# Kernel optimization log

Hardware: AMD Instinct MI355X
Metric: run time of the kernel (lower is better)

## Reference

```python
import jax, jax.numpy as jnp
import numpy as np

# --- fake-quant helpers (Brevitas INT quantization, straight-through in bwd) ---

def quant_weight_2bit(w):
    # symmetric signed 2-bit, narrow range: integer levels {-1, 0, 1}
    qmax = 1.0
    s = jnp.max(jnp.abs(jax.lax.stop_gradient(w))) / qmax
    r = jnp.clip(jnp.round(w / s), -qmax, qmax) * s
    return w + jax.lax.stop_gradient(r - w)  # STE


def quant_relu_2bit(x, max_val=6.0):
    # unsigned 2-bit activation quant: levels {0, 1, 2, 3} scaled to [0, max_val]
    n = 3.0  # 2**2 - 1
    s = max_val / n
    y = jnp.clip(x, 0.0, max_val)  # relu + clamp at max_val
    r = jnp.round(y / s) * s
    return y + jax.lax.stop_gradient(r - y)  # STE


def conv3x3_same(x, w):
    # NCHW input, OIHW weight, stride 1, padding 1
    return jax.lax.conv_general_dilated(
        x, w, window_strides=(1, 1), padding=((1, 1), (1, 1)),
        dimension_numbers=("NCHW", "OIHW", "NCHW"))


def maxpool2x2(x):
    return jax.lax.reduce_window(
        x, -jnp.inf, jax.lax.max,
        window_dimensions=(1, 1, 2, 2), window_strides=(1, 1, 2, 2),
        padding="VALID")


def setup_inputs() -> dict:
    key = jax.random.key(0)
    k0, k1, k2, k3 = jax.random.split(key, 4)
    B = 32768
    x = jax.random.normal(k0, (B, 1, 28, 28), dtype=jnp.float32)
    w1 = jax.random.normal(k1, (4, 1, 3, 3), dtype=jnp.float32) * 0.3
    w2 = jax.random.normal(k2, (4, 4, 3, 3), dtype=jnp.float32) * 0.2
    wf = jax.random.normal(k3, (10, 4 * 7 * 7), dtype=jnp.float32) * 0.1
    return {"x": x, "w1": w1, "w2": w2, "wf": wf}


def reference(x, w1, w2, wf):
    h = conv3x3_same(x, quant_weight_2bit(w1))        # [B,4,28,28]
    h = quant_relu_2bit(h)
    h = maxpool2x2(h)                                  # [B,4,14,14]
    h = conv3x3_same(h, quant_weight_2bit(w2))         # [B,4,14,14]
    h = quant_relu_2bit(h)
    h = maxpool2x2(h)                                  # [B,4,7,7]
    h = h.reshape(h.shape[0], -1)                      # [B,196]
    return h @ quant_weight_2bit(wf).T                 # [B,10]
```

## Files before the change

kernel.cpp:

```cpp
#include <hip/hip_runtime.h>

#define WSF_W1Q  0
#define WSF_SF2  36
#define WSI_W2P  0
#define WSI_L1   36
#define WSI_L3   37
#define WSI_L5   38
#define WSI_WFP  40

#define TOL 1e-4f

__device__ __forceinline__ int dot4(int a, int b, int c) {
#if __has_builtin(__builtin_amdgcn_sdot4)
    return __builtin_amdgcn_sdot4(a, b, c, false);
#else
    c += (int)(signed char)(a)       * (int)(signed char)(b);
    c += (int)(signed char)(a >> 8)  * (int)(signed char)(b >> 8);
    c += (int)(signed char)(a >> 16) * (int)(signed char)(b >> 16);
    c += (int)(signed char)(a >> 24) * (int)(signed char)(b >> 24);
    return c;
#endif
}

__global__ void qweights_kernel(const float* __restrict__ w1,
                                const float* __restrict__ w2,
                                const float* __restrict__ wf,
                                float* __restrict__ wsf) {
    int* wsi = (int*)wsf + 64;
    __shared__ float red[256];
    const int tid = threadIdx.x;

    float m = 0.f;
    for (int i = tid; i < 36; i += 256) m = fmaxf(m, fabsf(w1[i]));
    red[tid] = m; __syncthreads();
    for (int s = 128; s > 0; s >>= 1) { if (tid < s) red[tid] = fmaxf(red[tid], red[tid + s]); __syncthreads(); }
    const float s1 = red[0]; __syncthreads();

    m = 0.f;
    for (int i = tid; i < 144; i += 256) m = fmaxf(m, fabsf(w2[i]));
    red[tid] = m; __syncthreads();
    for (int s = 128; s > 0; s >>= 1) { if (tid < s) red[tid] = fmaxf(red[tid], red[tid + s]); __syncthreads(); }
    const float s2 = red[0]; __syncthreads();

    m = 0.f;
    for (int i = tid; i < 1960; i += 256) m = fmaxf(m, fabsf(wf[i]));
    red[tid] = m; __syncthreads();
    for (int s = 128; s > 0; s >>= 1) { if (tid < s) red[tid] = fmaxf(red[tid], red[tid + s]); __syncthreads(); }
    const float sf = red[0];

    for (int i = tid; i < 36; i += 256) {
        double l = rint((double)w1[i] / (double)s1);
        l = fmin(fmax(l, -1.0), 1.0);
        wsf[WSF_W1Q + i] = (float)(l * (double)s1);
    }
    for (int u = tid; u < 36; u += 256) {
        int oc = u / 9, tap = u - oc * 9;
        int dy = tap / 3, dx = tap - dy * 3;
        int v = 0;
        for (int ic = 0; ic < 4; ++ic) {
            double l = rint((double)w2[((oc * 4 + ic) * 3 + dy) * 3 + dx] / (double)s2);
            l = fmin(fmax(l, -1.0), 1.0);
            v |= ((int)l & 0xFF) << (8 * ic);
        }
        wsi[WSI_W2P + u] = v;
    }
    for (int u = tid; u < 64 * 12; u += 256) {
        int k4 = u / 12, o = u - k4 * 12;
        int v = 0;
        if (o < 10) {
            for (int b = 0; b < 4; ++b) {
                int k = 4 * k4 + b;
                if (k < 196) {
                    double l = rint((double)wf[o * 196 + k] / (double)sf);
                    l = fmin(fmax(l, -1.0), 1.0);
                    v |= ((int)l & 0xFF) << (8 * b);
                }
            }
        }
        wsi[WSI_WFP + u] = v;
    }
    if (tid == 0) {
        int L1 = 10000, L3 = 10000, L5 = 10000;
        for (int L = 108; L >= 0; --L) {
            double xv = 2.0 * (double)s2 * (double)L;
            double lv = rint(fmin(fmax(xv, 0.0), 6.0) * 0.5);
            if (lv >= 1.0) L1 = L;
            if (lv >= 2.0) L3 = L;
            if (lv >= 3.0) L5 = L;
        }
        wsi[WSI_L1] = L1; wsi[WSI_L3] = L3; wsi[WSI_L5] = L5;
        wsf[WSF_SF2] = 2.0f * sf;
    }
}

#define WAVES 4
#define P_IN 30
#define P_P1 18

__global__ __launch_bounds__(256, 8)
void fused_net_kernel(const float* __restrict__ x,
                      const float* __restrict__ wsf,
                      float* __restrict__ out, int B) {
    const int* wsi = (const int*)wsf + 64;

    __shared__ __align__(16) float s_in[WAVES][900];
    __shared__ __align__(16) int   s_p1[WAVES][16 * P_P1];
    __shared__ __align__(16) unsigned char s_p2[WAVES][256];

    const int tid  = threadIdx.x;
    const int wave = tid >> 6;
    const int lane = tid & 63;
    const int img  = blockIdx.x * WAVES + wave;
    const bool act = (img < B);

    float* in_p = s_in[wave];
    int*   p1i  = s_p1[wave];
    unsigned char* p2b = s_p2[wave];

    const float* w1 = wsf + WSF_W1Q;

    {
        float4 zf = make_float4(0.f, 0.f, 0.f, 0.f);
        float4* z1 = (float4*)in_p;
        for (int t = lane; t < 225; t += 64) z1[t] = zf;
        int4 zi = make_int4(0, 0, 0, 0);
        int4* z2 = (int4*)p1i;
        for (int t = lane; t < 72; t += 64) z2[t] = zi;
    }
    __syncthreads();

    if (act) {
        const float4* xv = (const float4*)(x + (size_t)img * 784);
        for (int t = lane; t < 196; t += 64) {
            float4 v = xv[t];
            int row = t / 7;
            int c   = (t - row * 7) * 4;
            float* dst = in_p + (row + 1) * P_IN + c + 1;
            dst[0] = v.x; dst[1] = v.y; dst[2] = v.z; dst[3] = v.w;
        }
    }
    __syncthreads();

    if (act) {
        for (int t = lane; t < 196; t += 64) {
            int i = t / 14, j = t - i * 14;
            const float* base = in_p + (2 * i) * P_IN + 2 * j;
            float d[4][4];
            #pragma unroll
            for (int r = 0; r < 4; ++r) {
                const float* rp = base + r * P_IN;
                float2 a = *(const float2*)rp;
                float2 b = *(const float2*)(rp + 2);
                d[r][0] = a.x; d[r][1] = a.y; d[r][2] = b.x; d[r][3] = b.y;
            }

            int lv[4];
            float chkmin = 1e9f;
            #pragma unroll
            for (int oc = 0; oc < 4; ++oc) {
                float a00 = 0.f, a01 = 0.f, a10 = 0.f, a11 = 0.f;
                #pragma unroll
                for (int r = 0; r < 3; ++r)
                    #pragma unroll
                    for (int c = 0; c < 3; ++c) {
                        float wv = w1[oc * 9 + r * 3 + c];
                        a00 = fmaf(wv, d[r][c],         a00);
                        a01 = fmaf(wv, d[r][c + 1],     a01);
                        a10 = fmaf(wv, d[r + 1][c],     a10);
                        a11 = fmaf(wv, d[r + 1][c + 1], a11);
                    }
                float mx = fmaxf(fmaxf(a00, a01), fmaxf(a10, a11));
                lv[oc] = (mx > 1.f) + (mx > 3.f) + (mx > 5.f);
                float d3 = fabsf(mx - 3.f);
                chkmin = fminf(chkmin, fminf(d3, fabsf(d3 - 2.f)));
            }
            if (chkmin < TOL) {
                double dd[4][4];
                #pragma unroll
                for (int r = 0; r < 4; ++r)
                    #pragma unroll
                    for (int c = 0; c < 4; ++c) dd[r][c] = (double)d[r][c];
                #pragma unroll
                for (int oc = 0; oc < 4; ++oc) {
                    double a00 = 0, a01 = 0, a10 = 0, a11 = 0;
                    #pragma unroll
                    for (int r = 0; r < 3; ++r)
                        #pragma unroll
                        for (int c = 0; c < 3; ++c) {
                            double wv = (double)w1[oc * 9 + r * 3 + c];
                            a00 = fma(wv, dd[r][c],         a00);
                            a01 = fma(wv, dd[r][c + 1],     a01);
                            a10 = fma(wv, dd[r + 1][c],     a10);
                            a11 = fma(wv, dd[r + 1][c + 1], a11);
                        }
                    double mx = fmax(fmax(a00, a01), fmax(a10, a11));
                    lv[oc] = (int)rint(fmin(fmax(mx, 0.0), 6.0) * 0.5);
                }
            }
            p1i[(i + 1) * P_P1 + (j + 1)] =
                lv[0] | (lv[1] << 8) | (lv[2] << 16) | (lv[3] << 24);
        }
    }
    __syncthreads();

    if (act) {
        const int ocl = lane & 3;
        int w2r[9];
        #pragma unroll
        for (int t = 0; t < 9; ++t) w2r[t] = wsi[WSI_W2P + ocl * 9 + t];
        const int L1 = wsi[WSI_L1], L3 = wsi[WSI_L3], L5 = wsi[WSI_L5];

        for (int u = lane; u < 196; u += 64) {
            int pix = u >> 2;
            int i = pix / 7, j = pix - 7 * i;
            const int* bp = p1i + (2 * i) * P_P1 + 2 * j;
            int d[4][4];
            #pragma unroll
            for (int r = 0; r < 4; ++r) {
                int2 a = *(const int2*)(bp + r * P_P1);
                int2 b = *(const int2*)(bp + r * P_P1 + 2);
                d[r][0] = a.x; d[r][1] = a.y; d[r][2] = b.x; d[r][3] = b.y;
            }
            int a00 = 0, a01 = 0, a10 = 0, a11 = 0;
            #pragma unroll
            for (int r = 0; r < 3; ++r)
                #pragma unroll
                for (int c = 0; c < 3; ++c) {
                    int wv = w2r[r * 3 + c];
                    a00 = dot4(d[r][c],         wv, a00);
                    a01 = dot4(d[r][c + 1],     wv, a01);
                    a10 = dot4(d[r + 1][c],     wv, a10);
                    a11 = dot4(d[r + 1][c + 1], wv, a11);
                }
            int mx = max(max(a00, a01), max(a10, a11));
            int lvq = (mx >= L1) + (mx >= L3) + (mx >= L5);
            p2b[ocl * 49 + pix] = (unsigned char)lvq;
        }
    }
    __syncthreads();

    if (act) {
        int acc[10];
        #pragma unroll
        for (int o = 0; o < 10; ++o) acc[o] = 0;
        if (lane < 49) {
            int h4 = ((const int*)p2b)[lane];
            const int* wr = wsi + WSI_WFP + lane * 12;
            #pragma unroll
            for (int o = 0; o < 10; ++o) acc[o] = dot4(h4, wr[o], acc[o]);
        }
        #pragma unroll
        for (int o = 0; o < 10; ++o) {
            #pragma unroll
            for (int off = 32; off > 0; off >>= 1)
                acc[o] += __shfl_xor(acc[o], off, 64);
        }
        if (lane == 0) {
            const float sf2 = wsf[WSF_SF2];
            float2* op = (float2*)(out + (size_t)img * 10);
            #pragma unroll
            for (int o = 0; o < 5; ++o)
                op[o] = make_float2(sf2 * (float)acc[2 * o],
                                    sf2 * (float)acc[2 * o + 1]);
        }
    }
}

extern "C" void kernel_launch(void* const* d_in, const int* in_sizes, int n_in,
                              void* d_out, int out_size, void* d_ws, size_t ws_size,
                              hipStream_t stream) {
    const float* x  = (const float*)d_in[0];
    const float* w1 = (const float*)d_in[1];
    const float* w2 = (const float*)d_in[2];
    const float* wf = (const float*)d_in[3];
    float* wsf = (float*)d_ws;
    float* out = (float*)d_out;

    const int B = in_sizes[0] / 784;

    qweights_kernel<<<1, 256, 0, stream>>>(w1, w2, wf, wsf);
    fused_net_kernel<<<(B + WAVES - 1) / WAVES, 256, 0, stream>>>(x, wsf, out, B);
}
```

Before: 210.1 us.

## Replace block barriers with per-wave LDS fences and pack reductions into 16-bit lanes

Each wave works on its own image in private shared-memory slices, so the block-wide barriers are replaced with lgkmcnt waits. Conv1 uses a fixed three-iteration loop plus a 16-lane tail that splits output channels across lanes. Conv2 is restructured so each of 49 lanes computes all four channels. The FC cross-lane reduction packs two outputs per 32-bit register with packed 16-bit adds, halving the shuffles. The weight prep kernel shrinks to a single wave using shuffle and ballot reductions. Risks: the LDS fences depend on wave-private data and on the implicit ordering of lanes within one wave, and the 16-bit packed sums must not overflow.

```diff
diff --git a/kernel.cpp b/kernel.cpp
--- a/kernel.cpp
+++ b/kernel.cpp
@@ -8,88 +8,82 @@
 #define WSI_L5   38
 #define WSI_WFP  40
 
-#define TOL 1e-4f
+#define TOL2 4e-5f
 
 __device__ __forceinline__ int dot4(int a, int b, int c) {
-#if __has_builtin(__builtin_amdgcn_sdot4)
     return __builtin_amdgcn_sdot4(a, b, c, false);
-#else
-    c += (int)(signed char)(a)       * (int)(signed char)(b);
-    c += (int)(signed char)(a >> 8)  * (int)(signed char)(b >> 8);
-    c += (int)(signed char)(a >> 16) * (int)(signed char)(b >> 16);
-    c += (int)(signed char)(a >> 24) * (int)(signed char)(b >> 24);
-    return c;
-#endif
-}
+}
+
+__device__ __forceinline__ int pk_add16(int a, int b) {
+    int r;
+    asm("v_pk_add_i16 %0, %1, %2" : "=v"(r) : "v"(a), "v"(b));
+    return r;
+}
+
+#define LDS_FENCE() asm volatile("s_waitcnt lgkmcnt(0)" ::: "memory")
 
 __global__ void qweights_kernel(const float* __restrict__ w1,
                                 const float* __restrict__ w2,
                                 const float* __restrict__ wf,
                                 float* __restrict__ wsf) {
     int* wsi = (int*)wsf + 64;
-    __shared__ float red[256];
-    const int tid = threadIdx.x;
-
-    float m = 0.f;
-    for (int i = tid; i < 36; i += 256) m = fmaxf(m, fabsf(w1[i]));
-    red[tid] = m; __syncthreads();
-    for (int s = 128; s > 0; s >>= 1) { if (tid < s) red[tid] = fmaxf(red[tid], red[tid + s]); __syncthreads(); }
-    const float s1 = red[0]; __syncthreads();
-
-    m = 0.f;
-    for (int i = tid; i < 144; i += 256) m = fmaxf(m, fabsf(w2[i]));
-    red[tid] = m; __syncthreads();
-    for (int s = 128; s > 0; s >>= 1) { if (tid < s) red[tid] = fmaxf(red[tid], red[tid + s]); __syncthreads(); }
-    const float s2 = red[0]; __syncthreads();
-
-    m = 0.f;
-    for (int i = tid; i < 1960; i += 256) m = fmaxf(m, fabsf(wf[i]));
-    red[tid] = m; __syncthreads();
-    for (int s = 128; s > 0; s >>= 1) { if (tid < s) red[tid] = fmaxf(red[tid], red[tid + s]); __syncthreads(); }
-    const float sf = red[0];
-
-    for (int i = tid; i < 36; i += 256) {
-        double l = rint((double)w1[i] / (double)s1);
+    const int lane = threadIdx.x;
+
+    float m1 = 0.f, m2 = 0.f, mf = 0.f;
+    if (lane < 36) m1 = fabsf(w1[lane]);
+    for (int i = lane; i < 144; i += 64)  m2 = fmaxf(m2, fabsf(w2[i]));
+    for (int i = lane; i < 1960; i += 64) mf = fmaxf(mf, fabsf(wf[i]));
+    #pragma unroll
+    for (int off = 32; off; off >>= 1) {
+        m1 = fmaxf(m1, __shfl_xor(m1, off, 64));
+        m2 = fmaxf(m2, __shfl_xor(m2, off, 64));
+        mf = fmaxf(mf, __shfl_xor(mf, off, 64));
+    }
+    const float s1 = m1, s2 = m2, sf = mf;
+
+    if (lane < 36) {
+        double l = rint((double)w1[lane] / (double)s1);
         l = fmin(fmax(l, -1.0), 1.0);
-        wsf[WSF_W1Q + i] = (float)(l * (double)s1);
-    }
-    for (int u = tid; u < 36; u += 256) {
-        int oc = u / 9, tap = u - oc * 9;
-        int dy = tap / 3, dx = tap - dy * 3;
+        wsf[WSF_W1Q + lane] = (float)(l * (double)s1);
+    }
+    if (lane < 36) {
+        int oc = lane / 9, tap = lane % 9;
+        int dy = tap / 3, dx = tap % 3;
         int v = 0;
         for (int ic = 0; ic < 4; ++ic) {
             double l = rint((double)w2[((oc * 4 + ic) * 3 + dy) * 3 + dx] / (double)s2);
             l = fmin(fmax(l, -1.0), 1.0);
             v |= ((int)l & 0xFF) << (8 * ic);
         }
-        wsi[WSI_W2P + u] = v;
-    }
-    for (int u = tid; u < 64 * 12; u += 256) {
-        int k4 = u / 12, o = u - k4 * 12;
+        wsi[WSI_W2P + lane] = v;
+    }
+    for (int u = lane; u < 49 * 12; u += 64) {
+        int pix = u / 12, o = u - 12 * pix;
         int v = 0;
         if (o < 10) {
             for (int b = 0; b < 4; ++b) {
-                int k = 4 * k4 + b;
-                if (k < 196) {
-                    double l = rint((double)wf[o * 196 + k] / (double)sf);
-                    l = fmin(fmax(l, -1.0), 1.0);
-                    v |= ((int)l & 0xFF) << (8 * b);
-                }
+                double l = rint((double)wf[o * 196 + b * 49 + pix] / (double)sf);
+                l = fmin(fmax(l, -1.0), 1.0);
+                v |= ((int)l & 0xFF) << (8 * b);
             }
         }
         wsi[WSI_WFP + u] = v;
     }
-    if (tid == 0) {
-        int L1 = 10000, L3 = 10000, L5 = 10000;
-        for (int L = 108; L >= 0; --L) {
-            double xv = 2.0 * (double)s2 * (double)L;
-            double lv = rint(fmin(fmax(xv, 0.0), 6.0) * 0.5);
-            if (lv >= 1.0) L1 = L;
-            if (lv >= 2.0) L3 = L;
-            if (lv >= 3.0) L5 = L;
-        }
-        wsi[WSI_L1] = L1; wsi[WSI_L3] = L3; wsi[WSI_L5] = L5;
-        wsf[WSF_SF2] = 2.0f * sf;
+    {
+        double xa = 2.0 * (double)s2 * (double)lane;
+        double xb = 2.0 * (double)s2 * (double)(lane + 64);
+        double la = rint(fmin(fmax(xa, 0.0), 6.0) * 0.5);
+        double lb = rint(fmin(fmax(xb, 0.0), 6.0) * 0.5);
+        unsigned long long b1a = __ballot(la >= 1.0), b1b = __ballot(lb >= 1.0);
+        unsigned long long b3a = __ballot(la >= 2.0), b3b = __ballot(lb >= 2.0);
+        unsigned long long b5a = __ballot(la >= 3.0), b5b = __ballot(lb >= 3.0);
+        if (lane == 0) {
+            int L1 = b1a ? __ffsll(b1a) - 1 : (b1b ? 64 + __ffsll(b1b) - 1 : 4096);
+            int L3 = b3a ? __ffsll(b3a) - 1 : (b3b ? 64 + __ffsll(b3b) - 1 : 4096);
+            int L5 = b5a ? __ffsll(b5a) - 1 : (b5b ? 64 + __ffsll(b5b) - 1 : 4096);
+            wsi[WSI_L1] = L1; wsi[WSI_L3] = L3; wsi[WSI_L5] = L5;
+            wsf[WSF_SF2] = 2.0f * sf;
+        }
     }
 }
 
@@ -105,7 +99,7 @@
 
     __shared__ __align__(16) float s_in[WAVES][900];
     __shared__ __align__(16) int   s_p1[WAVES][16 * P_P1];
-    __shared__ __align__(16) unsigned char s_p2[WAVES][256];
+    __shared__ __align__(16) int   s_p2[WAVES][52];
 
     const int tid  = threadIdx.x;
     const int wave = tid >> 6;
@@ -115,8 +109,7 @@
 
     float* in_p = s_in[wave];
     int*   p1i  = s_p1[wave];
-    unsigned char* p2b = s_p2[wave];
-
+    int*   p2i  = s_p2[wave];
     const float* w1 = wsf + WSF_W1Q;
 
     {
@@ -127,7 +120,7 @@
         int4* z2 = (int4*)p1i;
         for (int t = lane; t < 72; t += 64) z2[t] = zi;
     }
-    __syncthreads();
+    LDS_FENCE();
 
     if (act) {
         const float4* xv = (const float4*)(x + (size_t)img * 784);
@@ -139,23 +132,23 @@
             dst[0] = v.x; dst[1] = v.y; dst[2] = v.z; dst[3] = v.w;
         }
     }
-    __syncthreads();
+    LDS_FENCE();
 
     if (act) {
-        for (int t = lane; t < 196; t += 64) {
-            int i = t / 14, j = t - i * 14;
+        #pragma unroll 1
+        for (int it = 0; it < 3; ++it) {
+            const int t = lane + (it << 6);
+            const int i = t / 14, j = t - i * 14;
             const float* base = in_p + (2 * i) * P_IN + 2 * j;
             float d[4][4];
             #pragma unroll
             for (int r = 0; r < 4; ++r) {
-                const float* rp = base + r * P_IN;
-                float2 a = *(const float2*)rp;
-                float2 b = *(const float2*)(rp + 2);
+                float2 a = *(const float2*)(base + r * P_IN);
+                float2 b = *(const float2*)(base + r * P_IN + 2);
                 d[r][0] = a.x; d[r][1] = a.y; d[r][2] = b.x; d[r][3] = b.y;
             }
-
-            int lv[4];
-            float chkmin = 1e9f;
+            float rr[4];
+            float dmax = 0.f;
             #pragma unroll
             for (int oc = 0; oc < 4; ++oc) {
                 float a00 = 0.f, a01 = 0.f, a10 = 0.f, a11 = 0.f;
@@ -170,11 +163,12 @@
                         a11 = fmaf(wv, d[r + 1][c + 1], a11);
                     }
                 float mx = fmaxf(fmaxf(a00, a01), fmaxf(a10, a11));
-                lv[oc] = (mx > 1.f) + (mx > 3.f) + (mx > 5.f);
-                float d3 = fabsf(mx - 3.f);
-                chkmin = fminf(chkmin, fminf(d3, fabsf(d3 - 2.f)));
-            }
-            if (chkmin < TOL) {
+                float cc = fminf(fmaxf(0.5f * mx, 0.f), 3.f);
+                float rv = rintf(cc);
+                rr[oc] = rv;
+                dmax = fmaxf(dmax, fabsf(cc - rv));
+            }
+            if (dmax > 0.5f - TOL2) {
                 double dd[4][4];
                 #pragma unroll
                 for (int r = 0; r < 4; ++r)
@@ -194,74 +188,129 @@
                             a11 = fma(wv, dd[r + 1][c + 1], a11);
                         }
                     double mx = fmax(fmax(a00, a01), fmax(a10, a11));
-                    lv[oc] = (int)rint(fmin(fmax(mx, 0.0), 6.0) * 0.5);
+                    rr[oc] = (float)rint(fmin(fmax(0.5 * mx, 0.0), 3.0));
                 }
             }
             p1i[(i + 1) * P_P1 + (j + 1)] =
-                lv[0] | (lv[1] << 8) | (lv[2] << 16) | (lv[3] << 24);
-        }
-    }
-    __syncthreads();
-
-    if (act) {
-        const int ocl = lane & 3;
-        int w2r[9];
+                (int)rr[0] | ((int)rr[1] << 8) | ((int)rr[2] << 16) | ((int)rr[3] << 24);
+        }
+        if (lane < 16) {
+            const int px = 192 + (lane >> 2), oc = lane & 3;
+            const int i = 13, j = px - 182;
+            const float* base = in_p + (2 * i) * P_IN + 2 * j;
+            float d[4][4];
+            #pragma unroll
+            for (int r = 0; r < 4; ++r) {
+                float2 a = *(const float2*)(base + r * P_IN);
+                float2 b = *(const float2*)(base + r * P_IN + 2);
+                d[r][0] = a.x; d[r][1] = a.y; d[r][2] = b.x; d[r][3] = b.y;
+            }
+            const float* w9 = w1 + oc * 9;
+            float a00 = 0.f, a01 = 0.f, a10 = 0.f, a11 = 0.f;
+            #pragma unroll
+            for (int r = 0; r < 3; ++r)
+                #pragma unroll
+                for (int c = 0; c < 3; ++c) {
+                    float wv = w9[r * 3 + c];
+                    a00 = fmaf(wv, d[r][c],         a00);
+                    a01 = fmaf(wv, d[r][c + 1],     a01);
+                    a10 = fmaf(wv, d[r + 1][c],     a10);
+                    a11 = fmaf(wv, d[r + 1][c + 1], a11);
+                }
+            float mx = fmaxf(fmaxf(a00, a01), fmaxf(a10, a11));
+            float cc = fminf(fmaxf(0.5f * mx, 0.f), 3.f);
+            float rv = rintf(cc);
+            if (fabsf(cc - rv) > 0.5f - TOL2) {
+                double dd00 = 0, dd01 = 0, dd10 = 0, dd11 = 0;
+                #pragma unroll
+                for (int r = 0; r < 3; ++r)
+                    #pragma unroll
+                    for (int c = 0; c < 3; ++c) {
+                        double wv = (double)w9[r * 3 + c];
+                        dd00 = fma(wv, (double)d[r][c],         dd00);
+                        dd01 = fma(wv, (double)d[r][c + 1],     dd01);
+                        dd10 = fma(wv, (double)d[r + 1][c],     dd10);
+                        dd11 = fma(wv, (double)d[r + 1][c + 1], dd11);
+                    }
+                double mxd = fmax(fmax(dd00, dd01), fmax(dd10, dd11));
+                rv = (float)rint(fmin(fmax(0.5 * mxd, 0.0), 3.0));
+            }
+            int lv = (int)rv;
+            int v = lv | (__shfl_xor(lv, 1, 64) << 8);
+            v |= (__shfl_xor(v, 2, 64) << 16);
+            if ((lane & 3) == 0)
+                p1i[(i + 1) * P_P1 + (j + 1)] = v;
+        }
+    }
+    LDS_FENCE();
+
+    if (act && lane < 49) {
+        const int i = lane / 7, j = lane - 7 * i;
+        const int* bp = p1i + (2 * i) * P_P1 + 2 * j;
+        int d[4][4];
         #pragma unroll
-        for (int t = 0; t < 9; ++t) w2r[t] = wsi[WSI_W2P + ocl * 9 + t];
+        for (int r = 0; r < 4; ++r) {
+            int2 a = *(const int2*)(bp + r * P_P1);
+            int2 b = *(const int2*)(bp + r * P_P1 + 2);
+            d[r][0] = a.x; d[r][1] = a.y; d[r][2] = b.x; d[r][3] = b.y;
+        }
         const int L1 = wsi[WSI_L1], L3 = wsi[WSI_L3], L5 = wsi[WSI_L5];
-
-        for (int u = lane; u < 196; u += 64) {
-            int pix = u >> 2;
-            int i = pix / 7, j = pix - 7 * i;
-            const int* bp = p1i + (2 * i) * P_P1 + 2 * j;
-            int d[4][4];
-            #pragma unroll
-            for (int r = 0; r < 4; ++r) {
-                int2 a = *(const int2*)(bp + r * P_P1);
-                int2 b = *(const int2*)(bp + r * P_P1 + 2);
-                d[r][0] = a.x; d[r][1] = a.y; d[r][2] = b.x; d[r][3] = b.y;
-            }
+        int pk = 0;
+        #pragma unroll
+        for (int oc = 0; oc < 4; ++oc) {
             int a00 = 0, a01 = 0, a10 = 0, a11 = 0;
             #pragma unroll
             for (int r = 0; r < 3; ++r)
                 #pragma unroll
                 for (int c = 0; c < 3; ++c) {
-                    int wv = w2r[r * 3 + c];
+                    int wv = wsi[WSI_W2P + oc * 9 + r * 3 + c];
                     a00 = dot4(d[r][c],         wv, a00);
                     a01 = dot4(d[r][c + 1],     wv, a01);
                     a10 = dot4(d[r + 1][c],     wv, a10);
                     a11 = dot4(d[r + 1][c + 1], wv, a11);
                 }
             int mx = max(max(a00, a01), max(a10, a11));
-            int lvq = (mx >= L1) + (mx >= L3) + (mx >= L5);
-            p2b[ocl * 49 + pix] = (unsigned char)lvq;
-        }
-    }
-    __syncthreads();
+            int lv = (mx >= L1) + (mx >= L3) + (mx >= L5);
+            pk |= lv << (8 * oc);
+        }
+        p2i[lane] = pk;
+    }
+    LDS_FENCE();
 
     if (act) {
-        int acc[10];
+        int p[5] = {0, 0, 0, 0, 0};
+        if (lane < 49) {
+            int h4 = p2i[lane];
+            const int* wr = wsi + WSI_WFP + lane * 12;
+            int4 wa = *(const int4*)wr;
+            int4 wb = *(const int4*)(wr + 4);
+            int2 wc = *(const int2*)(wr + 8);
+            int a0 = dot4(h4, wa.x, 0), a1 = dot4(h4, wa.y, 0);
+            int a2 = dot4(h4, wa.z, 0), a3 = dot4(h4, wa.w, 0);
+            int a4 = dot4(h4, wb.x, 0), a5 = dot4(h4, wb.y, 0);
+            int a6 = dot4(h4, wb.z, 0), a7 = dot4(h4, wb.w, 0);
+            int a8 = dot4(h4, wc.x, 0), a9 = dot4(h4, wc.y, 0);
+            p[0] = (a0 << 16) | (a1 & 0xFFFF);
+            p[1] = (a2 << 16) | (a3 & 0xFFFF);
+            p[2] = (a4 << 16) | (a5 & 0xFFFF);
+            p[3] = (a6 << 16) | (a7 & 0xFFFF);
+            p[4] = (a8 << 16) | (a9 & 0xFFFF);
+        }
         #pragma unroll
-        for (int o = 0; o < 10; ++o) acc[o] = 0;
-        if (lane < 49) {
-            int h4 = ((const int*)p2b)[lane];
-            const int* wr = wsi + WSI_WFP + lane * 12;
-            #pragma unroll
-            for (int o = 0; o < 10; ++o) acc[o] = dot4(h4, wr[o], acc[o]);
-        }
-        #pragma unroll
-        for (int o = 0; o < 10; ++o) {
-            #pragma unroll
-            for (int off = 32; off > 0; off >>= 1)
-                acc[o] += __shfl_xor(acc[o], off, 64);
+        for (int off = 32; off; off >>= 1) {
+            #pragma unroll
+            for (int k = 0; k < 5; ++k)
+                p[k] = pk_add16(p[k], __shfl_xor(p[k], off, 64));
         }
         if (lane == 0) {
             const float sf2 = wsf[WSF_SF2];
             float2* op = (float2*)(out + (size_t)img * 10);
             #pragma unroll
-            for (int o = 0; o < 5; ++o)
-                op[o] = make_float2(sf2 * (float)acc[2 * o],
-                                    sf2 * (float)acc[2 * o + 1]);
+            for (int k = 0; k < 5; ++k) {
+                int hi = p[k] >> 16;
+                int lo = (int)(short)(p[k] & 0xFFFF);
+                op[k] = make_float2(sf2 * (float)hi, sf2 * (float)lo);
+            }
         }
     }
 }
@@ -278,6 +327,6 @@
 
     const int B = in_sizes[0] / 784;
 
-    qweights_kernel<<<1, 256, 0, stream>>>(w1, w2, wf, wsf);
+    qweights_kernel<<<1, 64, 0, stream>>>(w1, w2, wf, wsf);
     fused_net_kernel<<<(B + WAVES - 1) / WAVES, 256, 0, stream>>>(x, wsf, out, B);
 }
```

Measured after the change: 197.8 us. 5.8% less time.
